# Performance work log

Measured on AMD Instinct MI355X. Metric: run time of the kernel, lower is better.

Reference implementation:

```python
import jax, jax.numpy as jnp
import numpy as np

ALPHA = 1.0

def setup_inputs() -> dict:
    key = jax.random.key(0)
    k1, k2 = jax.random.split(key)
    x = jax.random.normal(k1, (65536, 512), dtype=jnp.float32)
    clusters = jax.random.normal(k2, (256, 512), dtype=jnp.float32)
    return {"x": x, "clusters": clusters}

def reference(x, clusters):
    # Squared Euclidean distance to each centroid via the GEMM expansion
    x2 = jnp.sum(x * x, axis=1, keepdims=True)            # (B, 1)
    c2 = jnp.sum(clusters * clusters, axis=1)             # (K,)
    cross = x @ clusters.T                                # (B, K) GEMM
    d2 = jnp.maximum(x2 + c2 - 2.0 * cross, 0.0)          # (B, K)
    # Student-t kernel (DEC soft assignment)
    q = 1.0 / (1.0 + d2 / ALPHA)
    q = q ** ((ALPHA + 1.0) / 2.0)
    q = q / jnp.sum(q, axis=1, keepdims=True)             # row-normalize
    return q
```

## Files before the change

### kernel.cpp

```cpp
#include <hip/hip_runtime.h>
#include <hip/hip_bf16.h>


typedef __attribute__((ext_vector_type(8))) short short8v;
typedef __attribute__((ext_vector_type(4))) float f32x4;

#define DDIM 512
#define KCL  256
#define BM   128
#define NT   512
#define NTILES 16
#define BTILE  8192

__device__ __forceinline__ short f2bf(float f) {
    __hip_bfloat16 h = __float2bfloat16(f);
    return __builtin_bit_cast(short, h);
}

__device__ __forceinline__ void glds16(const void* g, void* l) {
    __builtin_amdgcn_global_load_lds(
        (const __attribute__((address_space(1))) unsigned int*)g,
        (__attribute__((address_space(3))) unsigned int*)l, 16, 0, 0);
}

__global__ void prep(const float* __restrict__ cl, short* __restrict__ wsB,
                     float* __restrict__ wsC2) {
    const int t = threadIdx.x;
    if (blockIdx.x < 64) {
        const int u = blockIdx.x * 256 + t;
        const int img = u >> 10, gi = u & 1023;
        const int g = gi >> 6, lq = (gi >> 4) & 3, l15 = gi & 15;
        const float* src = cl + (size_t)(g * 16 + l15) * DDIM + img * 32 + lq * 8;
        float4 a = *(const float4*)src;
        float4 b = *(const float4*)(src + 4);
        short8v s;
        s[0]=f2bf(a.x); s[1]=f2bf(a.y); s[2]=f2bf(a.z); s[3]=f2bf(a.w);
        s[4]=f2bf(b.x); s[5]=f2bf(b.y); s[6]=f2bf(b.z); s[7]=f2bf(b.w);
        *(short8v*)&wsB[(size_t)u * 8] = s;
    } else {
        const int cidx = (blockIdx.x - 64) * 16 + (t >> 4);
        const int j = t & 15;
        const float* src = cl + (size_t)cidx * DDIM + j * 32;
        float s = 0.f;
#pragma unroll
        for (int i = 0; i < 8; ++i) {
            float4 v = ((const float4*)src)[i];
            s += v.x*v.x + v.y*v.y + v.z*v.z + v.w*v.w;
        }
        s += __shfl_xor(s, 1); s += __shfl_xor(s, 2);
        s += __shfl_xor(s, 4); s += __shfl_xor(s, 8);
        if (j == 0) wsC2[cidx] = s;
    }
}

#define SFENCE() __builtin_amdgcn_sched_barrier(0)
#define BARV4()  asm volatile("s_waitcnt vmcnt(4) lgkmcnt(0)\ns_barrier" ::: "memory")
#define BARV0()  asm volatile("s_waitcnt vmcnt(0) lgkmcnt(0)\ns_barrier" ::: "memory")

__global__ __launch_bounds__(NT, 4)
void dec_main(const float* __restrict__ x, const short* __restrict__ wsB,
              const float* __restrict__ wsC2, float* __restrict__ out) {
    __shared__ __align__(16) short lB3[3][BTILE];
    __shared__ __align__(16) short lA[2][4096];
    __shared__ float s_x2[BM];
    __shared__ float s_rs[4][BM];

    const int t = threadIdx.x, lane = t & 63, w = t >> 6;
    const int rg = w >> 2, cg = w & 3;
    const int l15 = lane & 15, lq = lane >> 4;
    const int row0 = blockIdx.x * BM;

    const int R = t >> 2, q = t & 3;
    const float* xs = x + (size_t)(row0 + R) * DDIM + q * 8;
    const int awr = ((R >> 4) * 64 + (((R & 15) ^ (2 * q)) + 16 * q)) * 8;
    const int aoff = (((l15 ^ (2 * lq)) + 16 * lq)) * 8;

    const short* bb = wsB;

    f32x4 acc[4][4];
#pragma unroll
    for (int m = 0; m < 4; ++m)
#pragma unroll
        for (int n = 0; n < 4; ++n) acc[m][n] = (f32x4){0.f,0.f,0.f,0.f};
    float x2p = 0.f;
    float4 XA0, XA1, XB0, XB1;

#define GLDS(TT, LBN)                                        \
    {  const short* src_ = bb + (size_t)(TT) * BTILE;        \
       glds16(src_ + t * 8,        (LBN) + t * 8);           \
       glds16(src_ + 4096 + t * 8, (LBN) + 4096 + t * 8); }

#define LOADX(TT, X0R, X1R)                                  \
    {  X0R = *(const float4*)(xs + (TT) * 32);               \
       X1R = *(const float4*)(xs + (TT) * 32 + 4); }

#define CVT(X0R, X1R, ABN)                                                       \
    {  short8v s_;                                                               \
       s_[0]=f2bf(X0R.x); s_[1]=f2bf(X0R.y); s_[2]=f2bf(X0R.z); s_[3]=f2bf(X0R.w);\
       s_[4]=f2bf(X1R.x); s_[5]=f2bf(X1R.y); s_[6]=f2bf(X1R.z); s_[7]=f2bf(X1R.w);\
       x2p += X0R.x*X0R.x + X0R.y*X0R.y + X0R.z*X0R.z + X0R.w*X0R.w              \
            + X1R.x*X1R.x + X1R.y*X1R.y + X1R.z*X1R.z + X1R.w*X1R.w;             \
       *(short8v*)&lA[ABN][awr] = s_; }

#define MSTEP(ABN, LBN)                                                          \
    {  short8v a0 = *(const short8v*)&lA[ABN][(rg*4+0)*512 + aoff];              \
       short8v a1 = *(const short8v*)&lA[ABN][(rg*4+1)*512 + aoff];              \
       short8v a2 = *(const short8v*)&lA[ABN][(rg*4+2)*512 + aoff];              \
       short8v a3 = *(const short8v*)&lA[ABN][(rg*4+3)*512 + aoff];              \
       short8v b0 = *(const short8v*)&(LBN)[cg*2048 + lane*8];                   \
       short8v b1 = *(const short8v*)&(LBN)[cg*2048 + 512  + lane*8];            \
       short8v b2 = *(const short8v*)&(LBN)[cg*2048 + 1024 + lane*8];            \
       short8v b3 = *(const short8v*)&(LBN)[cg*2048 + 1536 + lane*8];            \
       acc[0][0] = __builtin_amdgcn_mfma_f32_16x16x32_bf16(a0, b0, acc[0][0], 0,0,0); \
       acc[0][1] = __builtin_amdgcn_mfma_f32_16x16x32_bf16(a0, b1, acc[0][1], 0,0,0); \
       acc[0][2] = __builtin_amdgcn_mfma_f32_16x16x32_bf16(a0, b2, acc[0][2], 0,0,0); \
       acc[0][3] = __builtin_amdgcn_mfma_f32_16x16x32_bf16(a0, b3, acc[0][3], 0,0,0); \
       acc[1][0] = __builtin_amdgcn_mfma_f32_16x16x32_bf16(a1, b0, acc[1][0], 0,0,0); \
       acc[1][1] = __builtin_amdgcn_mfma_f32_16x16x32_bf16(a1, b1, acc[1][1], 0,0,0); \
       acc[1][2] = __builtin_amdgcn_mfma_f32_16x16x32_bf16(a1, b2, acc[1][2], 0,0,0); \
       acc[1][3] = __builtin_amdgcn_mfma_f32_16x16x32_bf16(a1, b3, acc[1][3], 0,0,0); \
       acc[2][0] = __builtin_amdgcn_mfma_f32_16x16x32_bf16(a2, b0, acc[2][0], 0,0,0); \
       acc[2][1] = __builtin_amdgcn_mfma_f32_16x16x32_bf16(a2, b1, acc[2][1], 0,0,0); \
       acc[2][2] = __builtin_amdgcn_mfma_f32_16x16x32_bf16(a2, b2, acc[2][2], 0,0,0); \
       acc[2][3] = __builtin_amdgcn_mfma_f32_16x16x32_bf16(a2, b3, acc[2][3], 0,0,0); \
       acc[3][0] = __builtin_amdgcn_mfma_f32_16x16x32_bf16(a3, b0, acc[3][0], 0,0,0); \
       acc[3][1] = __builtin_amdgcn_mfma_f32_16x16x32_bf16(a3, b1, acc[3][1], 0,0,0); \
       acc[3][2] = __builtin_amdgcn_mfma_f32_16x16x32_bf16(a3, b2, acc[3][2], 0,0,0); \
       acc[3][3] = __builtin_amdgcn_mfma_f32_16x16x32_bf16(a3, b3, acc[3][3], 0,0,0); }

#define ITER(J, ABC, ABN, BCUR, BNXT, XC0, XC1, XL0, XL1)                        \
    {  if ((J) + 2 < NTILES) { LOADX((J) + 2, XL0, XL1); }                       \
       SFENCE();                                                                 \
       if ((J) + 2 < NTILES) { GLDS((J) + 2, BNXT); }                            \
       SFENCE();                                                                 \
       if ((J) + 1 < NTILES) { CVT(XC0, XC1, ABN); }                             \
       MSTEP(ABC, BCUR);                                                         \
       SFENCE();                                                                 \
       if ((J) + 2 < NTILES) { BARV4(); }                                        \
       else if ((J) + 1 < NTILES) { BARV0(); }                                   \
       SFENCE(); }

    LOADX(0, XA0, XA1);  SFENCE();
    GLDS(0, &lB3[0][0]); SFENCE();
    LOADX(1, XB0, XB1);  SFENCE();
    GLDS(1, &lB3[1][0]); SFENCE();
    CVT(XA0, XA1, 0);
    SFENCE();
    BARV4();
    SFENCE();

    ITER( 0, 0, 1, &lB3[0][0], &lB3[2][0], XB0, XB1, XA0, XA1)
    ITER( 1, 1, 0, &lB3[1][0], &lB3[0][0], XA0, XA1, XB0, XB1)
    ITER( 2, 0, 1, &lB3[2][0], &lB3[1][0], XB0, XB1, XA0, XA1)
    ITER( 3, 1, 0, &lB3[0][0], &lB3[2][0], XA0, XA1, XB0, XB1)
    ITER( 4, 0, 1, &lB3[1][0], &lB3[0][0], XB0, XB1, XA0, XA1)
    ITER( 5, 1, 0, &lB3[2][0], &lB3[1][0], XA0, XA1, XB0, XB1)
    ITER( 6, 0, 1, &lB3[0][0], &lB3[2][0], XB0, XB1, XA0, XA1)
    ITER( 7, 1, 0, &lB3[1][0], &lB3[0][0], XA0, XA1, XB0, XB1)
    ITER( 8, 0, 1, &lB3[2][0], &lB3[1][0], XB0, XB1, XA0, XA1)
    ITER( 9, 1, 0, &lB3[0][0], &lB3[2][0], XA0, XA1, XB0, XB1)
    ITER(10, 0, 1, &lB3[1][0], &lB3[0][0], XB0, XB1, XA0, XA1)
    ITER(11, 1, 0, &lB3[2][0], &lB3[1][0], XA0, XA1, XB0, XB1)
    ITER(12, 0, 1, &lB3[0][0], &lB3[2][0], XB0, XB1, XA0, XA1)
    ITER(13, 1, 0, &lB3[1][0], &lB3[0][0], XA0, XA1, XB0, XB1)
    ITER(14, 0, 1, &lB3[2][0], &lB3[1][0], XB0, XB1, XA0, XA1)
    ITER(15, 1, 0, &lB3[0][0], &lB3[2][0], XA0, XA1, XB0, XB1)

    x2p += __shfl_xor(x2p, 1); x2p += __shfl_xor(x2p, 2);
    if (q == 0) s_x2[R] = x2p;
    __syncthreads();

    float c2a[4];
#pragma unroll
    for (int n = 0; n < 4; ++n) c2a[n] = wsC2[cg*64 + n*16 + l15];

#pragma unroll
    for (int m = 0; m < 4; ++m)
#pragma unroll
        for (int n = 0; n < 4; ++n)
#pragma unroll
            for (int r = 0; r < 4; ++r) {
                const int rw = rg*64 + m*16 + lq*4 + r;
                float d2 = fmaxf(s_x2[rw] + c2a[n] - 2.0f * acc[m][n][r], 0.0f);
                acc[m][n][r] = 1.0f / (1.0f + d2);
            }

#pragma unroll
    for (int m = 0; m < 4; ++m)
#pragma unroll
        for (int r = 0; r < 4; ++r) {
            float p = acc[m][0][r] + acc[m][1][r] + acc[m][2][r] + acc[m][3][r];
            p += __shfl_xor(p, 1); p += __shfl_xor(p, 2);
            p += __shfl_xor(p, 4); p += __shfl_xor(p, 8);
            if (l15 == 0) s_rs[cg][rg*64 + m*16 + lq*4 + r] = p;
        }
    __syncthreads();

#pragma unroll
    for (int m = 0; m < 4; ++m)
#pragma unroll
        for (int r = 0; r < 4; ++r) {
            const int rw = rg*64 + m*16 + lq*4 + r;
            const float rinv = 1.0f / (s_rs[0][rw] + s_rs[1][rw] + s_rs[2][rw] + s_rs[3][rw]);
            float* o = out + (size_t)(row0 + rw) * KCL + cg*64 + l15;
#pragma unroll
            for (int n = 0; n < 4; ++n)
                o[n * 16] = acc[m][n][r] * rinv;
        }
}

extern "C" void kernel_launch(void* const* d_in, const int* in_sizes, int n_in,
                              void* d_out, int out_size, void* d_ws, size_t ws_size,
                              hipStream_t stream) {
    const float* x  = (const float*)d_in[0];
    const float* cl = (const float*)d_in[1];
    float* out = (float*)d_out;
    short* wsB  = (short*)d_ws;
    float* wsC2 = (float*)((char*)d_ws + (size_t)NTILES * BTILE * sizeof(short));

    prep<<<80, 256, 0, stream>>>(cl, wsB, wsC2);
    const int B = in_sizes[0] / DDIM;
    dec_main<<<B / BM, NT, 0, stream>>>(x, wsB, wsC2, out);
}
```

Baseline: 49.18 us.

## Process two K-tiles per pipeline stage with single-buffered A and aliased epilogue smem

The main loop now handles 64 columns of x per iteration, running two MFMA half-steps against two B tiles from a four-buffer ring, so the count of barrier-synchronised iterations drops from 16 to 8. The A tile becomes a single buffer that is written after an LDS-drain barrier, and the epilogue scratch arrays alias the B buffers. The goal is fewer barriers and less synchronisation overhead per unit of MFMA work. In exchange, the prefetch is shallower: the loop waits on vmcnt(0) every iteration, and LDS use per block rises to 80 KB, which may reduce occupancy below the four blocks per CU the launch bounds request.

```diff
diff --git a/kernel.cpp b/kernel.cpp
--- a/kernel.cpp
+++ b/kernel.cpp
@@ -9,8 +9,8 @@
 #define KCL  256
 #define BM   128
 #define NT   512
-#define NTILES 16
-#define BTILE  8192
+#define NIMG 16
+#define BTILE 8192
 
 __device__ __forceinline__ short f2bf(float f) {
     __hip_bfloat16 h = __float2bfloat16(f);
@@ -53,17 +53,17 @@
     }
 }
 
-#define SFENCE() __builtin_amdgcn_sched_barrier(0)
-#define BARV4()  asm volatile("s_waitcnt vmcnt(4) lgkmcnt(0)\ns_barrier" ::: "memory")
-#define BARV0()  asm volatile("s_waitcnt vmcnt(0) lgkmcnt(0)\ns_barrier" ::: "memory")
+#define SFENCE()  __builtin_amdgcn_sched_barrier(0)
+#define BARLGKM() asm volatile("s_waitcnt lgkmcnt(0)\ns_barrier" ::: "memory")
+#define BARV0()   asm volatile("s_waitcnt vmcnt(0) lgkmcnt(0)\ns_barrier" ::: "memory")
 
 __global__ __launch_bounds__(NT, 4)
 void dec_main(const float* __restrict__ x, const short* __restrict__ wsB,
               const float* __restrict__ wsC2, float* __restrict__ out) {
-    __shared__ __align__(16) short lB3[3][BTILE];
-    __shared__ __align__(16) short lA[2][4096];
-    __shared__ float s_x2[BM];
-    __shared__ float s_rs[4][BM];
+    __shared__ __align__(16) short lB4[4][BTILE];
+    __shared__ __align__(16) short lA[8192];
+    float* const s_x2 = (float*)&lB4[0][0];
+    float* const s_rs = ((float*)&lB4[0][0]) + BM;
 
     const int t = threadIdx.x, lane = t & 63, w = t >> 6;
     const int rg = w >> 2, cg = w & 3;
@@ -71,11 +71,9 @@
     const int row0 = blockIdx.x * BM;
 
     const int R = t >> 2, q = t & 3;
-    const float* xs = x + (size_t)(row0 + R) * DDIM + q * 8;
-    const int awr = ((R >> 4) * 64 + (((R & 15) ^ (2 * q)) + 16 * q)) * 8;
-    const int aoff = (((l15 ^ (2 * lq)) + 16 * lq)) * 8;
-
-    const short* bb = wsB;
+    const float* xs = x + (size_t)(row0 + R) * DDIM + q * 16;
+    const int kk = q >> 1, lqa = (q & 1) * 2;
+    const int awr0 = kk * 4096 + (R >> 4) * 512 + ((R & 15) + 16 * lqa) * 8;
 
     f32x4 acc[4][4];
 #pragma unroll
@@ -83,34 +81,41 @@
 #pragma unroll
         for (int n = 0; n < 4; ++n) acc[m][n] = (f32x4){0.f,0.f,0.f,0.f};
     float x2p = 0.f;
-    float4 XA0, XA1, XB0, XB1;
-
-#define GLDS(TT, LBN)                                        \
-    {  const short* src_ = bb + (size_t)(TT) * BTILE;        \
-       glds16(src_ + t * 8,        (LBN) + t * 8);           \
-       glds16(src_ + 4096 + t * 8, (LBN) + 4096 + t * 8); }
-
-#define LOADX(TT, X0R, X1R)                                  \
-    {  X0R = *(const float4*)(xs + (TT) * 32);               \
-       X1R = *(const float4*)(xs + (TT) * 32 + 4); }
-
-#define CVT(X0R, X1R, ABN)                                                       \
-    {  short8v s_;                                                               \
-       s_[0]=f2bf(X0R.x); s_[1]=f2bf(X0R.y); s_[2]=f2bf(X0R.z); s_[3]=f2bf(X0R.w);\
-       s_[4]=f2bf(X1R.x); s_[5]=f2bf(X1R.y); s_[6]=f2bf(X1R.z); s_[7]=f2bf(X1R.w);\
-       x2p += X0R.x*X0R.x + X0R.y*X0R.y + X0R.z*X0R.z + X0R.w*X0R.w              \
-            + X1R.x*X1R.x + X1R.y*X1R.y + X1R.z*X1R.z + X1R.w*X1R.w;             \
-       *(short8v*)&lA[ABN][awr] = s_; }
-
-#define MSTEP(ABN, LBN)                                                          \
-    {  short8v a0 = *(const short8v*)&lA[ABN][(rg*4+0)*512 + aoff];              \
-       short8v a1 = *(const short8v*)&lA[ABN][(rg*4+1)*512 + aoff];              \
-       short8v a2 = *(const short8v*)&lA[ABN][(rg*4+2)*512 + aoff];              \
-       short8v a3 = *(const short8v*)&lA[ABN][(rg*4+3)*512 + aoff];              \
-       short8v b0 = *(const short8v*)&(LBN)[cg*2048 + lane*8];                   \
-       short8v b1 = *(const short8v*)&(LBN)[cg*2048 + 512  + lane*8];            \
-       short8v b2 = *(const short8v*)&(LBN)[cg*2048 + 1024 + lane*8];            \
-       short8v b3 = *(const short8v*)&(LBN)[cg*2048 + 1536 + lane*8];            \
+    float4 Xa0, Xa1, Xa2, Xa3;
+
+#define GLDS(TT, BUFI)                                               \
+    {  const short* src_ = wsB + (size_t)(TT) * BTILE;               \
+       glds16(src_ + t * 8,        &lB4[BUFI][0] + t * 8);           \
+       glds16(src_ + 4096 + t * 8, &lB4[BUFI][0] + 4096 + t * 8); }
+
+#define LOADX(SLAB)                                                  \
+    {  Xa0 = *(const float4*)(xs + (SLAB) * 64);                     \
+       Xa1 = *(const float4*)(xs + (SLAB) * 64 + 4);                 \
+       Xa2 = *(const float4*)(xs + (SLAB) * 64 + 8);                 \
+       Xa3 = *(const float4*)(xs + (SLAB) * 64 + 12); }
+
+#define CVT()                                                                    \
+    {  short8v s0, s1;                                                           \
+       s0[0]=f2bf(Xa0.x); s0[1]=f2bf(Xa0.y); s0[2]=f2bf(Xa0.z); s0[3]=f2bf(Xa0.w);\
+       s0[4]=f2bf(Xa1.x); s0[5]=f2bf(Xa1.y); s0[6]=f2bf(Xa1.z); s0[7]=f2bf(Xa1.w);\
+       s1[0]=f2bf(Xa2.x); s1[1]=f2bf(Xa2.y); s1[2]=f2bf(Xa2.z); s1[3]=f2bf(Xa2.w);\
+       s1[4]=f2bf(Xa3.x); s1[5]=f2bf(Xa3.y); s1[6]=f2bf(Xa3.z); s1[7]=f2bf(Xa3.w);\
+       x2p += Xa0.x*Xa0.x + Xa0.y*Xa0.y + Xa0.z*Xa0.z + Xa0.w*Xa0.w              \
+            + Xa1.x*Xa1.x + Xa1.y*Xa1.y + Xa1.z*Xa1.z + Xa1.w*Xa1.w              \
+            + Xa2.x*Xa2.x + Xa2.y*Xa2.y + Xa2.z*Xa2.z + Xa2.w*Xa2.w              \
+            + Xa3.x*Xa3.x + Xa3.y*Xa3.y + Xa3.z*Xa3.z + Xa3.w*Xa3.w;             \
+       *(short8v*)&lA[awr0]       = s0;                                          \
+       *(short8v*)&lA[awr0 + 128] = s1; }
+
+#define MHALF(CC, BUFI)                                                          \
+    {  short8v a0 = *(const short8v*)&lA[(CC)*4096 + (rg*4+0)*512 + lane*8];     \
+       short8v a1 = *(const short8v*)&lA[(CC)*4096 + (rg*4+1)*512 + lane*8];     \
+       short8v a2 = *(const short8v*)&lA[(CC)*4096 + (rg*4+2)*512 + lane*8];     \
+       short8v a3 = *(const short8v*)&lA[(CC)*4096 + (rg*4+3)*512 + lane*8];     \
+       short8v b0 = *(const short8v*)&lB4[BUFI][cg*2048 + lane*8];               \
+       short8v b1 = *(const short8v*)&lB4[BUFI][cg*2048 + 512  + lane*8];        \
+       short8v b2 = *(const short8v*)&lB4[BUFI][cg*2048 + 1024 + lane*8];        \
+       short8v b3 = *(const short8v*)&lB4[BUFI][cg*2048 + 1536 + lane*8];        \
        acc[0][0] = __builtin_amdgcn_mfma_f32_16x16x32_bf16(a0, b0, acc[0][0], 0,0,0); \
        acc[0][1] = __builtin_amdgcn_mfma_f32_16x16x32_bf16(a0, b1, acc[0][1], 0,0,0); \
        acc[0][2] = __builtin_amdgcn_mfma_f32_16x16x32_bf16(a0, b2, acc[0][2], 0,0,0); \
@@ -128,43 +133,33 @@
        acc[3][2] = __builtin_amdgcn_mfma_f32_16x16x32_bf16(a3, b2, acc[3][2], 0,0,0); \
        acc[3][3] = __builtin_amdgcn_mfma_f32_16x16x32_bf16(a3, b3, acc[3][3], 0,0,0); }
 
-#define ITER(J, ABC, ABN, BCUR, BNXT, XC0, XC1, XL0, XL1)                        \
-    {  if ((J) + 2 < NTILES) { LOADX((J) + 2, XL0, XL1); }                       \
+#define ITER(J, C0, C1, N0, N1)                                                  \
+    {  if ((J) + 1 < 8) { LOADX((J) + 1); }                                      \
        SFENCE();                                                                 \
-       if ((J) + 2 < NTILES) { GLDS((J) + 2, BNXT); }                            \
+       if ((J) < 7) { GLDS(2*(J)+2, N0); GLDS(2*(J)+3, N1); }                    \
        SFENCE();                                                                 \
-       if ((J) + 1 < NTILES) { CVT(XC0, XC1, ABN); }                             \
-       MSTEP(ABC, BCUR);                                                         \
-       SFENCE();                                                                 \
-       if ((J) + 2 < NTILES) { BARV4(); }                                        \
-       else if ((J) + 1 < NTILES) { BARV0(); }                                   \
+       MHALF(0, C0);                                                             \
+       MHALF(1, C1);                                                             \
+       BARLGKM();                                                                \
+       if ((J) + 1 < 8) { CVT(); }                                               \
+       if ((J) < 7) { BARV0(); }                                                 \
        SFENCE(); }
 
-    LOADX(0, XA0, XA1);  SFENCE();
-    GLDS(0, &lB3[0][0]); SFENCE();
-    LOADX(1, XB0, XB1);  SFENCE();
-    GLDS(1, &lB3[1][0]); SFENCE();
-    CVT(XA0, XA1, 0);
+    LOADX(0);  SFENCE();
+    GLDS(0, 0); GLDS(1, 1);  SFENCE();
+    CVT();
     SFENCE();
-    BARV4();
+    BARV0();
     SFENCE();
 
-    ITER( 0, 0, 1, &lB3[0][0], &lB3[2][0], XB0, XB1, XA0, XA1)
-    ITER( 1, 1, 0, &lB3[1][0], &lB3[0][0], XA0, XA1, XB0, XB1)
-    ITER( 2, 0, 1, &lB3[2][0], &lB3[1][0], XB0, XB1, XA0, XA1)
-    ITER( 3, 1, 0, &lB3[0][0], &lB3[2][0], XA0, XA1, XB0, XB1)
-    ITER( 4, 0, 1, &lB3[1][0], &lB3[0][0], XB0, XB1, XA0, XA1)
-    ITER( 5, 1, 0, &lB3[2][0], &lB3[1][0], XA0, XA1, XB0, XB1)
-    ITER( 6, 0, 1, &lB3[0][0], &lB3[2][0], XB0, XB1, XA0, XA1)
-    ITER( 7, 1, 0, &lB3[1][0], &lB3[0][0], XA0, XA1, XB0, XB1)
-    ITER( 8, 0, 1, &lB3[2][0], &lB3[1][0], XB0, XB1, XA0, XA1)
-    ITER( 9, 1, 0, &lB3[0][0], &lB3[2][0], XA0, XA1, XB0, XB1)
-    ITER(10, 0, 1, &lB3[1][0], &lB3[0][0], XB0, XB1, XA0, XA1)
-    ITER(11, 1, 0, &lB3[2][0], &lB3[1][0], XA0, XA1, XB0, XB1)
-    ITER(12, 0, 1, &lB3[0][0], &lB3[2][0], XB0, XB1, XA0, XA1)
-    ITER(13, 1, 0, &lB3[1][0], &lB3[0][0], XA0, XA1, XB0, XB1)
-    ITER(14, 0, 1, &lB3[2][0], &lB3[1][0], XB0, XB1, XA0, XA1)
-    ITER(15, 1, 0, &lB3[0][0], &lB3[2][0], XA0, XA1, XB0, XB1)
+    ITER(0, 0, 1, 2, 3)
+    ITER(1, 2, 3, 0, 1)
+    ITER(2, 0, 1, 2, 3)
+    ITER(3, 2, 3, 0, 1)
+    ITER(4, 0, 1, 2, 3)
+    ITER(5, 2, 3, 0, 1)
+    ITER(6, 0, 1, 2, 3)
+    ITER(7, 2, 3, 0, 1)
 
     x2p += __shfl_xor(x2p, 1); x2p += __shfl_xor(x2p, 2);
     if (q == 0) s_x2[R] = x2p;
@@ -192,7 +187,7 @@
             float p = acc[m][0][r] + acc[m][1][r] + acc[m][2][r] + acc[m][3][r];
             p += __shfl_xor(p, 1); p += __shfl_xor(p, 2);
             p += __shfl_xor(p, 4); p += __shfl_xor(p, 8);
-            if (l15 == 0) s_rs[cg][rg*64 + m*16 + lq*4 + r] = p;
+            if (l15 == 0) s_rs[cg*BM + rg*64 + m*16 + lq*4 + r] = p;
         }
     __syncthreads();
 
@@ -201,7 +196,8 @@
 #pragma unroll
         for (int r = 0; r < 4; ++r) {
             const int rw = rg*64 + m*16 + lq*4 + r;
-            const float rinv = 1.0f / (s_rs[0][rw] + s_rs[1][rw] + s_rs[2][rw] + s_rs[3][rw]);
+            const float rinv = 1.0f / (s_rs[rw] + s_rs[BM + rw]
+                                     + s_rs[2*BM + rw] + s_rs[3*BM + rw]);
             float* o = out + (size_t)(row0 + rw) * KCL + cg*64 + l15;
 #pragma unroll
             for (int n = 0; n < 4; ++n)
@@ -216,7 +212,7 @@
     const float* cl = (const float*)d_in[1];
     float* out = (float*)d_out;
     short* wsB  = (short*)d_ws;
-    float* wsC2 = (float*)((char*)d_ws + (size_t)NTILES * BTILE * sizeof(short));
+    float* wsC2 = (float*)((char*)d_ws + (size_t)NIMG * BTILE * sizeof(short));
 
     prep<<<80, 256, 0, stream>>>(cl, wsB, wsC2);
     const int B = in_sizes[0] / DDIM;
```

New measurement: 76.98 us. 1.57x slower.

## Fuse centroid prep into main kernel, loading fp32 centroids and converting in-loop

Applied to the files above, without the earlier changes.

Removes the separate prep kernel that converted centroids to a bf16 swizzled layout and computed their squared norms. The main kernel now streams raw fp32 centroid tiles into LDS with a swizzled double buffer, converts them to bf16 right before the MFMAs, and accumulates the centroid norms in one row-group of waves. This saves a kernel launch and its dependency, but doubles the LDS traffic for B, adds conversion work to every block, and drops the B pipeline from triple to double buffering.

```diff
diff --git a/kernel.cpp b/kernel.cpp
--- a/kernel.cpp
+++ b/kernel.cpp
@@ -10,7 +10,6 @@
 #define BM   128
 #define NT   512
 #define NTILES 16
-#define BTILE  8192
 
 __device__ __forceinline__ short f2bf(float f) {
     __hip_bfloat16 h = __float2bfloat16(f);
@@ -23,47 +22,18 @@
         (__attribute__((address_space(3))) unsigned int*)l, 16, 0, 0);
 }
 
-__global__ void prep(const float* __restrict__ cl, short* __restrict__ wsB,
-                     float* __restrict__ wsC2) {
-    const int t = threadIdx.x;
-    if (blockIdx.x < 64) {
-        const int u = blockIdx.x * 256 + t;
-        const int img = u >> 10, gi = u & 1023;
-        const int g = gi >> 6, lq = (gi >> 4) & 3, l15 = gi & 15;
-        const float* src = cl + (size_t)(g * 16 + l15) * DDIM + img * 32 + lq * 8;
-        float4 a = *(const float4*)src;
-        float4 b = *(const float4*)(src + 4);
-        short8v s;
-        s[0]=f2bf(a.x); s[1]=f2bf(a.y); s[2]=f2bf(a.z); s[3]=f2bf(a.w);
-        s[4]=f2bf(b.x); s[5]=f2bf(b.y); s[6]=f2bf(b.z); s[7]=f2bf(b.w);
-        *(short8v*)&wsB[(size_t)u * 8] = s;
-    } else {
-        const int cidx = (blockIdx.x - 64) * 16 + (t >> 4);
-        const int j = t & 15;
-        const float* src = cl + (size_t)cidx * DDIM + j * 32;
-        float s = 0.f;
-#pragma unroll
-        for (int i = 0; i < 8; ++i) {
-            float4 v = ((const float4*)src)[i];
-            s += v.x*v.x + v.y*v.y + v.z*v.z + v.w*v.w;
-        }
-        s += __shfl_xor(s, 1); s += __shfl_xor(s, 2);
-        s += __shfl_xor(s, 4); s += __shfl_xor(s, 8);
-        if (j == 0) wsC2[cidx] = s;
-    }
-}
-
 #define SFENCE() __builtin_amdgcn_sched_barrier(0)
-#define BARV4()  asm volatile("s_waitcnt vmcnt(4) lgkmcnt(0)\ns_barrier" ::: "memory")
+#define BARV2()  asm volatile("s_waitcnt vmcnt(2) lgkmcnt(0)\ns_barrier" ::: "memory")
 #define BARV0()  asm volatile("s_waitcnt vmcnt(0) lgkmcnt(0)\ns_barrier" ::: "memory")
 
 __global__ __launch_bounds__(NT, 4)
-void dec_main(const float* __restrict__ x, const short* __restrict__ wsB,
-              const float* __restrict__ wsC2, float* __restrict__ out) {
-    __shared__ __align__(16) short lB3[3][BTILE];
+void dec_main(const float* __restrict__ x, const float* __restrict__ cl,
+              float* __restrict__ out) {
     __shared__ __align__(16) short lA[2][4096];
-    __shared__ float s_x2[BM];
-    __shared__ float s_rs[4][BM];
+    __shared__ __align__(16) float lBf[2][8192];
+    float* const s_x2 = (float*)&lA[0][0];
+    float* const s_rs = (float*)&lA[0][0] + BM;
+    float* const s_c2 = (float*)&lA[0][0] + BM + 4*BM;
 
     const int t = threadIdx.x, lane = t & 63, w = t >> 6;
     const int rg = w >> 2, cg = w & 3;
@@ -72,10 +42,18 @@
 
     const int R = t >> 2, q = t & 3;
     const float* xs = x + (size_t)(row0 + R) * DDIM + q * 8;
-    const int awr = ((R >> 4) * 64 + (((R & 15) ^ (2 * q)) + 16 * q)) * 8;
+    const int awr  = ((R >> 4) * 64 + (((R & 15) ^ (2 * q)) + 16 * q)) * 8;
     const int aoff = (((l15 ^ (2 * lq)) + 16 * lq)) * 8;
 
-    const short* bb = wsB;
+    int boff[4];
+#pragma unroll
+    for (int r = 0; r < 4; ++r) {
+        const int s  = t + r * 512;
+        const int cc = (s & 7) ^ ((s >> 3) & 7);
+        const int col = ((s >> 7) << 4) + ((s >> 3) & 15);
+        boff[r] = col * DDIM + ((cc >> 1) << 3) + ((cc & 1) << 2);
+    }
+    const int bo0 = l15 * 8 + ((lq * 2) ^ (l15 & 7));
 
     f32x4 acc[4][4];
 #pragma unroll
@@ -83,12 +61,15 @@
 #pragma unroll
         for (int n = 0; n < 4; ++n) acc[m][n] = (f32x4){0.f,0.f,0.f,0.f};
     float x2p = 0.f;
+    float c2p[4] = {0.f, 0.f, 0.f, 0.f};
     float4 XA0, XA1, XB0, XB1;
 
-#define GLDS(TT, LBN)                                        \
-    {  const short* src_ = bb + (size_t)(TT) * BTILE;        \
-       glds16(src_ + t * 8,        (LBN) + t * 8);           \
-       glds16(src_ + 4096 + t * 8, (LBN) + 4096 + t * 8); }
+#define GLDSB(TT, P)                                                 \
+    {  const float* im_ = cl + (TT) * 32;                            \
+       glds16(im_ + boff[0], &lBf[P][t * 4]);                        \
+       glds16(im_ + boff[1], &lBf[P][t * 4 + 2048]);                 \
+       glds16(im_ + boff[2], &lBf[P][t * 4 + 4096]);                 \
+       glds16(im_ + boff[3], &lBf[P][t * 4 + 6144]); }
 
 #define LOADX(TT, X0R, X1R)                                  \
     {  X0R = *(const float4*)(xs + (TT) * 32);               \
@@ -102,77 +83,81 @@
             + X1R.x*X1R.x + X1R.y*X1R.y + X1R.z*X1R.z + X1R.w*X1R.w;             \
        *(short8v*)&lA[ABN][awr] = s_; }
 
-#define MSTEP(ABN, LBN)                                                          \
+#define MSTEP(ABN, BP)                                                           \
     {  short8v a0 = *(const short8v*)&lA[ABN][(rg*4+0)*512 + aoff];              \
        short8v a1 = *(const short8v*)&lA[ABN][(rg*4+1)*512 + aoff];              \
        short8v a2 = *(const short8v*)&lA[ABN][(rg*4+2)*512 + aoff];              \
        short8v a3 = *(const short8v*)&lA[ABN][(rg*4+3)*512 + aoff];              \
-       short8v b0 = *(const short8v*)&(LBN)[cg*2048 + lane*8];                   \
-       short8v b1 = *(const short8v*)&(LBN)[cg*2048 + 512  + lane*8];            \
-       short8v b2 = *(const short8v*)&(LBN)[cg*2048 + 1024 + lane*8];            \
-       short8v b3 = *(const short8v*)&(LBN)[cg*2048 + 1536 + lane*8];            \
-       acc[0][0] = __builtin_amdgcn_mfma_f32_16x16x32_bf16(a0, b0, acc[0][0], 0,0,0); \
-       acc[0][1] = __builtin_amdgcn_mfma_f32_16x16x32_bf16(a0, b1, acc[0][1], 0,0,0); \
-       acc[0][2] = __builtin_amdgcn_mfma_f32_16x16x32_bf16(a0, b2, acc[0][2], 0,0,0); \
-       acc[0][3] = __builtin_amdgcn_mfma_f32_16x16x32_bf16(a0, b3, acc[0][3], 0,0,0); \
-       acc[1][0] = __builtin_amdgcn_mfma_f32_16x16x32_bf16(a1, b0, acc[1][0], 0,0,0); \
-       acc[1][1] = __builtin_amdgcn_mfma_f32_16x16x32_bf16(a1, b1, acc[1][1], 0,0,0); \
-       acc[1][2] = __builtin_amdgcn_mfma_f32_16x16x32_bf16(a1, b2, acc[1][2], 0,0,0); \
-       acc[1][3] = __builtin_amdgcn_mfma_f32_16x16x32_bf16(a1, b3, acc[1][3], 0,0,0); \
-       acc[2][0] = __builtin_amdgcn_mfma_f32_16x16x32_bf16(a2, b0, acc[2][0], 0,0,0); \
-       acc[2][1] = __builtin_amdgcn_mfma_f32_16x16x32_bf16(a2, b1, acc[2][1], 0,0,0); \
-       acc[2][2] = __builtin_amdgcn_mfma_f32_16x16x32_bf16(a2, b2, acc[2][2], 0,0,0); \
-       acc[2][3] = __builtin_amdgcn_mfma_f32_16x16x32_bf16(a2, b3, acc[2][3], 0,0,0); \
-       acc[3][0] = __builtin_amdgcn_mfma_f32_16x16x32_bf16(a3, b0, acc[3][0], 0,0,0); \
-       acc[3][1] = __builtin_amdgcn_mfma_f32_16x16x32_bf16(a3, b1, acc[3][1], 0,0,0); \
-       acc[3][2] = __builtin_amdgcn_mfma_f32_16x16x32_bf16(a3, b2, acc[3][2], 0,0,0); \
-       acc[3][3] = __builtin_amdgcn_mfma_f32_16x16x32_bf16(a3, b3, acc[3][3], 0,0,0); }
-
-#define ITER(J, ABC, ABN, BCUR, BNXT, XC0, XC1, XL0, XL1)                        \
+       _Pragma("unroll")                                                         \
+       for (int n = 0; n < 4; ++n) {                                             \
+           const int s0 = (cg*4 + n) * 128 + bo0;                                \
+           float4 blo = *(const float4*)&lBf[BP][s0 * 4];                        \
+           float4 bhi = *(const float4*)&lBf[BP][(s0 ^ 1) * 4];                  \
+           short8v bf_;                                                          \
+           bf_[0]=f2bf(blo.x); bf_[1]=f2bf(blo.y); bf_[2]=f2bf(blo.z); bf_[3]=f2bf(blo.w); \
+           bf_[4]=f2bf(bhi.x); bf_[5]=f2bf(bhi.y); bf_[6]=f2bf(bhi.z); bf_[7]=f2bf(bhi.w); \
+           if (rg == 0)                                                          \
+               c2p[n] += blo.x*blo.x + blo.y*blo.y + blo.z*blo.z + blo.w*blo.w   \
+                       + bhi.x*bhi.x + bhi.y*bhi.y + bhi.z*bhi.z + bhi.w*bhi.w;  \
+           acc[0][n] = __builtin_amdgcn_mfma_f32_16x16x32_bf16(a0, bf_, acc[0][n], 0,0,0); \
+           acc[1][n] = __builtin_amdgcn_mfma_f32_16x16x32_bf16(a1, bf_, acc[1][n], 0,0,0); \
+           acc[2][n] = __builtin_amdgcn_mfma_f32_16x16x32_bf16(a2, bf_, acc[2][n], 0,0,0); \
+           acc[3][n] = __builtin_amdgcn_mfma_f32_16x16x32_bf16(a3, bf_, acc[3][n], 0,0,0); \
+       } }
+
+#define ITER(J, ABC, ABN, XC0, XC1, XL0, XL1)                                    \
     {  if ((J) + 2 < NTILES) { LOADX((J) + 2, XL0, XL1); }                       \
        SFENCE();                                                                 \
-       if ((J) + 2 < NTILES) { GLDS((J) + 2, BNXT); }                            \
+       if ((J) + 1 < NTILES) { GLDSB((J) + 1, ((J) + 1) & 1); }                  \
        SFENCE();                                                                 \
        if ((J) + 1 < NTILES) { CVT(XC0, XC1, ABN); }                             \
-       MSTEP(ABC, BCUR);                                                         \
+       MSTEP(ABC, (J) & 1);                                                      \
        SFENCE();                                                                 \
-       if ((J) + 2 < NTILES) { BARV4(); }                                        \
+       if ((J) + 2 < NTILES) { BARV2(); }                                        \
        else if ((J) + 1 < NTILES) { BARV0(); }                                   \
        SFENCE(); }
 
     LOADX(0, XA0, XA1);  SFENCE();
-    GLDS(0, &lB3[0][0]); SFENCE();
+    GLDSB(0, 0);         SFENCE();
     LOADX(1, XB0, XB1);  SFENCE();
-    GLDS(1, &lB3[1][0]); SFENCE();
     CVT(XA0, XA1, 0);
     SFENCE();
-    BARV4();
+    BARV2();
     SFENCE();
 
-    ITER( 0, 0, 1, &lB3[0][0], &lB3[2][0], XB0, XB1, XA0, XA1)
-    ITER( 1, 1, 0, &lB3[1][0], &lB3[0][0], XA0, XA1, XB0, XB1)
-    ITER( 2, 0, 1, &lB3[2][0], &lB3[1][0], XB0, XB1, XA0, XA1)
-    ITER( 3, 1, 0, &lB3[0][0], &lB3[2][0], XA0, XA1, XB0, XB1)
-    ITER( 4, 0, 1, &lB3[1][0], &lB3[0][0], XB0, XB1, XA0, XA1)
-    ITER( 5, 1, 0, &lB3[2][0], &lB3[1][0], XA0, XA1, XB0, XB1)
-    ITER( 6, 0, 1, &lB3[0][0], &lB3[2][0], XB0, XB1, XA0, XA1)
-    ITER( 7, 1, 0, &lB3[1][0], &lB3[0][0], XA0, XA1, XB0, XB1)
-    ITER( 8, 0, 1, &lB3[2][0], &lB3[1][0], XB0, XB1, XA0, XA1)
-    ITER( 9, 1, 0, &lB3[0][0], &lB3[2][0], XA0, XA1, XB0, XB1)
-    ITER(10, 0, 1, &lB3[1][0], &lB3[0][0], XB0, XB1, XA0, XA1)
-    ITER(11, 1, 0, &lB3[2][0], &lB3[1][0], XA0, XA1, XB0, XB1)
-    ITER(12, 0, 1, &lB3[0][0], &lB3[2][0], XB0, XB1, XA0, XA1)
-    ITER(13, 1, 0, &lB3[1][0], &lB3[0][0], XA0, XA1, XB0, XB1)
-    ITER(14, 0, 1, &lB3[2][0], &lB3[1][0], XB0, XB1, XA0, XA1)
-    ITER(15, 1, 0, &lB3[0][0], &lB3[2][0], XA0, XA1, XB0, XB1)
+    ITER( 0, 0, 1, XB0, XB1, XA0, XA1)
+    ITER( 1, 1, 0, XA0, XA1, XB0, XB1)
+    ITER( 2, 0, 1, XB0, XB1, XA0, XA1)
+    ITER( 3, 1, 0, XA0, XA1, XB0, XB1)
+    ITER( 4, 0, 1, XB0, XB1, XA0, XA1)
+    ITER( 5, 1, 0, XA0, XA1, XB0, XB1)
+    ITER( 6, 0, 1, XB0, XB1, XA0, XA1)
+    ITER( 7, 1, 0, XA0, XA1, XB0, XB1)
+    ITER( 8, 0, 1, XB0, XB1, XA0, XA1)
+    ITER( 9, 1, 0, XA0, XA1, XB0, XB1)
+    ITER(10, 0, 1, XB0, XB1, XA0, XA1)
+    ITER(11, 1, 0, XA0, XA1, XB0, XB1)
+    ITER(12, 0, 1, XB0, XB1, XA0, XA1)
+    ITER(13, 1, 0, XA0, XA1, XB0, XB1)
+    ITER(14, 0, 1, XB0, XB1, XA0, XA1)
+    ITER(15, 1, 0, XA0, XA1, XB0, XB1)
+
+    __syncthreads();
 
     x2p += __shfl_xor(x2p, 1); x2p += __shfl_xor(x2p, 2);
     if (q == 0) s_x2[R] = x2p;
+
+#pragma unroll
+    for (int n = 0; n < 4; ++n) {
+        float v = c2p[n];
+        v += __shfl_xor(v, 16); v += __shfl_xor(v, 32);
+        if (rg == 0 && lq == 0) s_c2[cg*64 + n*16 + l15] = v;
+    }
     __syncthreads();
 
     float c2a[4];
 #pragma unroll
-    for (int n = 0; n < 4; ++n) c2a[n] = wsC2[cg*64 + n*16 + l15];
+    for (int n = 0; n < 4; ++n) c2a[n] = s_c2[cg*64 + n*16 + l15];
 
 #pragma unroll
     for (int m = 0; m < 4; ++m)
@@ -192,7 +177,7 @@
             float p = acc[m][0][r] + acc[m][1][r] + acc[m][2][r] + acc[m][3][r];
             p += __shfl_xor(p, 1); p += __shfl_xor(p, 2);
             p += __shfl_xor(p, 4); p += __shfl_xor(p, 8);
-            if (l15 == 0) s_rs[cg][rg*64 + m*16 + lq*4 + r] = p;
+            if (l15 == 0) s_rs[cg*BM + rg*64 + m*16 + lq*4 + r] = p;
         }
     __syncthreads();
 
@@ -201,7 +186,8 @@
 #pragma unroll
         for (int r = 0; r < 4; ++r) {
             const int rw = rg*64 + m*16 + lq*4 + r;
-            const float rinv = 1.0f / (s_rs[0][rw] + s_rs[1][rw] + s_rs[2][rw] + s_rs[3][rw]);
+            const float rinv = 1.0f / (s_rs[rw] + s_rs[BM + rw]
+                                     + s_rs[2*BM + rw] + s_rs[3*BM + rw]);
             float* o = out + (size_t)(row0 + rw) * KCL + cg*64 + l15;
 #pragma unroll
             for (int n = 0; n < 4; ++n)
@@ -215,10 +201,6 @@
     const float* x  = (const float*)d_in[0];
     const float* cl = (const float*)d_in[1];
     float* out = (float*)d_out;
-    short* wsB  = (short*)d_ws;
-    float* wsC2 = (float*)((char*)d_ws + (size_t)NTILES * BTILE * sizeof(short));
-
-    prep<<<80, 256, 0, stream>>>(cl, wsB, wsC2);
     const int B = in_sizes[0] / DDIM;
-    dec_main<<<B / BM, NT, 0, stream>>>(x, wsB, wsC2, out);
-}
+    dec_main<<<B / BM, NT, 0, stream>>>(x, cl, out);
+}
```

New measurement: 195.9 us. 298% more time.
